# Kernel tuning notes

Measured on AMD Instinct MI355X. Metric: run time of the kernel, lower is better.

The kernel has to match this reference:

```python
import jax, jax.numpy as jnp
import numpy as np
import math

DIM = 512


def setup_inputs() -> dict:
    key = jax.random.key(0)
    ks = jax.random.split(key, 6)
    B, N, D = 4, 4096, DIM
    H = D // 2
    features = jax.random.normal(ks[0], (B, N, D), dtype=jnp.float32)
    W1 = jax.random.normal(ks[1], (D, H), dtype=jnp.float32) * 0.02
    b1 = jnp.zeros((H,), dtype=jnp.float32)
    ln_g = jnp.ones((H,), dtype=jnp.float32)
    ln_b = jnp.zeros((H,), dtype=jnp.float32)
    W2 = jax.random.normal(ks[2], (H, 1), dtype=jnp.float32) * 0.02
    b2 = jnp.zeros((1,), dtype=jnp.float32)
    target_entropy = jnp.ones((1,), dtype=jnp.float32) * math.log(D)
    temperature = jnp.ones((1,), dtype=jnp.float32)
    return {"features": features, "W1": W1, "b1": b1, "ln_g": ln_g,
            "ln_b": ln_b, "W2": W2, "b2": b2,
            "target_entropy": target_entropy, "temperature": temperature}


def _layernorm(x, g, b, eps=1e-5):
    mu = jnp.mean(x, axis=-1, keepdims=True)
    var = jnp.mean((x - mu) ** 2, axis=-1, keepdims=True)
    return (x - mu) * jax.lax.rsqrt(var + eps) * g + b


def reference(features, W1, b1, ln_g, ln_b, W2, b2, target_entropy, temperature):
    # ---- compute_entropy: pairwise RBF kernel over [B, N, D] ----
    sq = jnp.sum(features ** 2, axis=-1)                       # [B, N]
    gram = jnp.einsum('bnd,bmd->bnm', features, features)      # [B, N, N]
    d2 = jnp.maximum(sq[:, :, None] + sq[:, None, :] - 2.0 * gram, 0.0)
    tau = temperature[0]
    kernel = jnp.exp(-d2 / (2.0 * tau ** 2))                   # [B, N, N]
    probs = kernel / jnp.sum(kernel, axis=-1, keepdims=True)
    entropy = -jnp.sum(probs * jnp.log(probs + 1e-6), axis=-1)  # [B, N]

    # ---- entropy estimator MLP (computed in original forward, output unused) ----
    h = features @ W1 + b1
    h = _layernorm(h, ln_g, ln_b)
    h = jax.nn.gelu(h, approximate=False)
    estimated_entropy = h @ W2 + b2                            # [B, N, 1] (unused)
    del estimated_entropy

    # ---- sigmoid-gated control signal ----
    entropy_diff = entropy - target_entropy[0]
    control_signal = jax.nn.sigmoid(-entropy_diff / tau)       # [B, N]
    controlled_features = features * control_signal[..., None]
    return controlled_features, control_signal
```

## Files before the change

### kernel.cpp

```cpp
#include <hip/hip_runtime.h>
#include <stdint.h>

#define N_TOK 4096
#define DIM   512
#define BATCH 4
#define BN    (BATCH * N_TOK)
#define NSUP  16
#define NPAIR 136
#define IPW   64
#define IPB   256
#define NG2   16
#define SPG   2
#define NSP   (NG2 / SPG)

typedef __attribute__((ext_vector_type(4))) float f32x4;
typedef __attribute__((ext_vector_type(8))) int   i32x8;

typedef const __attribute__((address_space(1))) uint32_t* gptr_t;
typedef __attribute__((address_space(3))) uint32_t* lptr_t;

__device__ __forceinline__ float sumsq8(uint lo, uint hi) {
    float s = 0.f, f;
    f = __builtin_amdgcn_cvt_f32_fp8((int)lo, 0); s = fmaf(f, f, s);
    f = __builtin_amdgcn_cvt_f32_fp8((int)lo, 1); s = fmaf(f, f, s);
    f = __builtin_amdgcn_cvt_f32_fp8((int)lo, 2); s = fmaf(f, f, s);
    f = __builtin_amdgcn_cvt_f32_fp8((int)lo, 3); s = fmaf(f, f, s);
    f = __builtin_amdgcn_cvt_f32_fp8((int)hi, 0); s = fmaf(f, f, s);
    f = __builtin_amdgcn_cvt_f32_fp8((int)hi, 1); s = fmaf(f, f, s);
    f = __builtin_amdgcn_cvt_f32_fp8((int)hi, 2); s = fmaf(f, f, s);
    f = __builtin_amdgcn_cvt_f32_fp8((int)hi, 3); s = fmaf(f, f, s);
    return s;
}

__global__ __launch_bounds__(256) void prep_kernel(
    const float* __restrict__ feat, uint8_t* __restrict__ fbT,
    float* __restrict__ sq)
{
    __shared__ __align__(16) long lt[1024];
    const int t = threadIdx.x;
    const int row16 = t >> 4, seg = t & 15;
    const size_t grp = blockIdx.x;
    const size_t row = grp * 16 + row16;

    const float4* src = (const float4*)(feat + row * DIM + seg * 32);
    uint32_t wd[8];
    float s = 0.f;
#pragma unroll
    for (int i = 0; i < 4; ++i) {
        float4 a = src[2 * i], b = src[2 * i + 1];
        uint lo = (uint)__builtin_amdgcn_cvt_pk_fp8_f32(a.x, a.y, 0, false);
        lo      = (uint)__builtin_amdgcn_cvt_pk_fp8_f32(a.z, a.w, (int)lo, true);
        uint hi = (uint)__builtin_amdgcn_cvt_pk_fp8_f32(b.x, b.y, 0, false);
        hi      = (uint)__builtin_amdgcn_cvt_pk_fp8_f32(b.z, b.w, (int)hi, true);
        wd[2 * i] = lo; wd[2 * i + 1] = hi;
        s += sumsq8(lo, hi);
    }

#pragma unroll
    for (int i = 0; i < 4; ++i) {
        int c = seg * 4 + i;
        long d = ((long)(unsigned)wd[2 * i + 1] << 32) | (unsigned)wd[2 * i];
        lt[c * 16 + ((row16 + c) & 15)] = d;
    }

#pragma unroll
    for (int m = 1; m < 16; m <<= 1) s += __shfl_xor(s, m);
    if (seg == 0) sq[row] = s;

    __syncthreads();
    long* ot = (long*)(fbT + grp * 8192);
#pragma unroll
    for (int i = 0; i < 4; ++i) {
        int p    = t + i * 256;
        int kk   = p >> 8;
        int rem  = p & 255;
        int half = rem >> 7;
        int l6   = (rem >> 1) & 63;
        int qq   = l6 >> 4;
        int r    = l6 & 15;
        int w8   = half * 2 + (p & 1);
        int c    = kk * 16 + qq * 4 + w8;
        ot[p] = lt[c * 16 + ((r + c) & 15)];
    }
}

__global__ __launch_bounds__(256, 2) void entropy_kernel(
    const uint8_t* __restrict__ fbT,
    const float* __restrict__ sq, const float* __restrict__ temp,
    float* __restrict__ Sp, float* __restrict__ Tp)
{
    __shared__ uint4 buf[2][1024];
    __shared__ float sqlds[256];
    __shared__ float sjS[4][256];
    __shared__ float sjT[4][256];
    const int t    = threadIdx.x;
    const int w    = t >> 6;
    const int lane = t & 63;
    const int q    = lane >> 4;
    const int c16  = lane & 15;
    const int lbo  = lane * 16;

    const int flat  = blockIdx.x;
    const int batch = flat / NPAIR;
    int rem = flat - batch * NPAIR;
    int aa = 0;
    while (rem >= NSUP - aa) { rem -= NSUP - aa; ++aa; }
    const int bb = aa + rem;
    const int iw    = aa * IPB + w * IPW;
    const int jbase = bb * IPB;
    const size_t rowbase = (size_t)batch * N_TOK;

    const float tau    = temp[0];
    const float inv2t2 = 0.5f / (tau * tau);
    const float cg_    = 1.0f / (tau * tau);

#pragma unroll
    for (int i = 0; i < 4; ++i) { sjS[w][lane * 4 + i] = 0.f; sjT[w][lane * 4 + i] = 0.f; }

    i32x8 afrag[4][4];
#pragma unroll
    for (int s = 0; s < 4; ++s) {
        const uint8_t* ga = fbT + ((rowbase + iw) / 16 + s) * 8192;
#pragma unroll
        for (int kk = 0; kk < 4; ++kk) {
            uint4 lo = *(const uint4*)(ga + kk * 2048 + lbo);
            uint4 hi = *(const uint4*)(ga + kk * 2048 + 1024 + lbo);
            i32x8 v = {(int)lo.x, (int)lo.y, (int)lo.z, (int)lo.w,
                       (int)hi.x, (int)hi.y, (int)hi.z, (int)hi.w};
            afrag[s][kk] = v;
        }
    }
    float pi_[4][4];
    float pim = -1e30f;
#pragma unroll
    for (int s = 0; s < 4; ++s) {
        float4 p4 = *(const float4*)(sq + rowbase + iw + s * 16 + q * 4);
        pi_[s][0] = -p4.x * inv2t2; pi_[s][1] = -p4.y * inv2t2;
        pi_[s][2] = -p4.z * inv2t2; pi_[s][3] = -p4.w * inv2t2;
        pim = fmaxf(pim, fmaxf(fmaxf(pi_[s][0], pi_[s][1]),
                               fmaxf(pi_[s][2], pi_[s][3])));
    }
    sqlds[t] = sq[rowbase + jbase + t];

    float S[4][4], T[4][4];
#pragma unroll
    for (int s = 0; s < 4; ++s)
#pragma unroll
        for (int r = 0; r < 4; ++r) { S[s][r] = 0.f; T[s][r] = 0.f; }

    const uint8_t* bgbase = fbT
        + ((size_t)batch * (N_TOK / 16) + (size_t)(jbase / 16)) * 8192;

    auto stage_sp = [&](int sp, int b) {
#pragma unroll
        for (int i = 0; i < SPG; ++i) {
            const uint8_t* gs = bgbase + ((size_t)sp * SPG + i) * 8192 + w * 2048 + lbo;
            uint8_t* ld = (uint8_t*)(&buf[b][0]) + i * 8192 + w * 2048;
            __builtin_amdgcn_global_load_lds((gptr_t)(const void*)gs,
                                             (lptr_t)(void*)ld, 16, 0, 0);
            __builtin_amdgcn_global_load_lds((gptr_t)(const void*)(gs + 1024),
                                             (lptr_t)(void*)(ld + 1024), 16, 0, 0);
        }
    };

    stage_sp(0, 0);
    stage_sp(1, 1);
    asm volatile("s_waitcnt lgkmcnt(0)" ::: "memory");
    __builtin_amdgcn_s_barrier();

    for (int sp = 0; sp < NSP; ++sp) {
        if (sp < NSP - 1) asm volatile("s_waitcnt vmcnt(4)" ::: "memory");
        else              asm volatile("s_waitcnt vmcnt(0)" ::: "memory");
        __builtin_amdgcn_s_barrier();
        __builtin_amdgcn_sched_barrier(0);

        const uint8_t* sb = (const uint8_t*)(&buf[sp & 1][0]);
        __builtin_amdgcn_s_setprio(1);
#pragma unroll
        for (int i = 0; i < SPG; ++i) {
            const int g = sp * SPG + i;
            const uint8_t* bs = sb + i * 8192;
            float pj = -sqlds[g * 16 + c16] * inv2t2;
            f32x4 acc[4] = {{0,0,0,0},{0,0,0,0},{0,0,0,0},{0,0,0,0}};
#pragma unroll
            for (int kk = 0; kk < 4; ++kk) {
                uint4 lo = *(const uint4*)(bs + kk * 2048 + lbo);
                uint4 hi = *(const uint4*)(bs + kk * 2048 + 1024 + lbo);
                i32x8 b = {(int)lo.x, (int)lo.y, (int)lo.z, (int)lo.w,
                           (int)hi.x, (int)hi.y, (int)hi.z, (int)hi.w};
                acc[0] = __builtin_amdgcn_mfma_scale_f32_16x16x128_f8f6f4(afrag[0][kk], b, acc[0], 0, 0, 0, 127, 0, 127);
                acc[1] = __builtin_amdgcn_mfma_scale_f32_16x16x128_f8f6f4(afrag[1][kk], b, acc[1], 0, 0, 0, 127, 0, 127);
                acc[2] = __builtin_amdgcn_mfma_scale_f32_16x16x128_f8f6f4(afrag[2][kk], b, acc[2], 0, 0, 0, 127, 0, 127);
                acc[3] = __builtin_amdgcn_mfma_scale_f32_16x16x128_f8f6f4(afrag[3][kk], b, acc[3], 0, 0, 0, 127, 0, 127);
            }
            float m0 = fmaxf(fmaxf(acc[0][0], acc[0][1]), fmaxf(acc[0][2], acc[0][3]));
            float m1 = fmaxf(fmaxf(acc[1][0], acc[1][1]), fmaxf(acc[1][2], acc[1][3]));
            float m2 = fmaxf(fmaxf(acc[2][0], acc[2][1]), fmaxf(acc[2][2], acc[2][3]));
            float m3 = fmaxf(fmaxf(acc[3][0], acc[3][1]), fmaxf(acc[3][2], acc[3][3]));
            float mm = fmaxf(fmaxf(m0, m1), fmaxf(m2, m3));
            float bound = fmaf(mm, cg_, pim + pj);
            if (__any(bound > -110.0f)) {
                float ks = 0.f, kt = 0.f;
#pragma unroll
                for (int s = 0; s < 4; ++s)
#pragma unroll
                    for (int r = 0; r < 4; ++r) {
                        float e   = fmaf(acc[s][r], cg_, pi_[s][r] + pj);
                        float ee  = fminf(e, 0.f);
                        float k   = __expf(ee);
                        float kei = k * ee;
                        S[s][r] += k;  T[s][r] += kei;
                        ks      += k;  kt      += kei;
                    }
                if (aa != bb) {
                    ks += __shfl_xor(ks, 16); ks += __shfl_xor(ks, 32);
                    kt += __shfl_xor(kt, 16); kt += __shfl_xor(kt, 32);
                    if (lane < 16) {
                        sjS[w][g * 16 + lane] = ks;
                        sjT[w][g * 16 + lane] = kt;
                    }
                }
            }
        }
        __builtin_amdgcn_s_setprio(0);

        asm volatile("s_waitcnt lgkmcnt(0)" ::: "memory");
        __builtin_amdgcn_s_barrier();
        __builtin_amdgcn_sched_barrier(0);
        if (sp + 2 < NSP) stage_sp(sp + 2, sp & 1);
    }

#pragma unroll
    for (int m = 1; m < 16; m <<= 1)
#pragma unroll
        for (int s = 0; s < 4; ++s)
#pragma unroll
            for (int r = 0; r < 4; ++r) {
                S[s][r] += __shfl_xor(S[s][r], m);
                T[s][r] += __shfl_xor(T[s][r], m);
            }
    if (c16 == 0) {
#pragma unroll
        for (int s = 0; s < 4; ++s)
#pragma unroll
            for (int r = 0; r < 4; ++r) {
                size_t idx = (size_t)bb * BN + rowbase + iw + s * 16 + q * 4 + r;
                Sp[idx] = S[s][r];
                Tp[idx] = T[s][r];
            }
    }

    if (aa != bb) {
        __syncthreads();
        float s4 = sjS[0][t] + sjS[1][t] + sjS[2][t] + sjS[3][t];
        float t4 = sjT[0][t] + sjT[1][t] + sjT[2][t] + sjT[3][t];
        size_t idx = (size_t)aa * BN + rowbase + jbase + t;
        Sp[idx] = s4;
        Tp[idx] = t4;
    }
}

__global__ __launch_bounds__(256) void finalize_kernel(
    const float* __restrict__ feat, const float* __restrict__ Sp,
    const float* __restrict__ Tp, const float* __restrict__ tgt,
    const float* __restrict__ temp, float* __restrict__ out)
{
    int row  = (blockIdx.x << 2) + (threadIdx.x >> 6);
    int lane = threadIdx.x & 63;
    float S = 0.0f, T = 0.0f;
#pragma unroll
    for (int j = 0; j < NSUP; ++j) {
        S += Sp[(size_t)j * BN + row];
        T += Tp[(size_t)j * BN + row];
    }
    float tau = temp[0];
    float E  = __logf(S) - T / S;
    float cs = 1.0f / (1.0f + __expf((E - tgt[0]) / tau));

    const float4* F4 = (const float4*)(feat + (size_t)row * DIM);
    float4*       O4 = (float4*)(out + (size_t)row * DIM);
    float4 v0 = F4[lane], v1 = F4[lane + 64];
    v0.x *= cs; v0.y *= cs; v0.z *= cs; v0.w *= cs;
    v1.x *= cs; v1.y *= cs; v1.z *= cs; v1.w *= cs;
    O4[lane] = v0; O4[lane + 64] = v1;
    if (lane == 0) out[(size_t)BN * DIM + row] = cs;
}

extern "C" void kernel_launch(void* const* d_in, const int* in_sizes, int n_in,
                              void* d_out, int out_size, void* d_ws, size_t ws_size,
                              hipStream_t stream) {
    const float* feat = (const float*)d_in[0];
    const float* tgt  = (const float*)d_in[7];
    const float* temp = (const float*)d_in[8];
    float* out = (float*)d_out;

    char* ws = (char*)d_ws;
    uint8_t* fbT = (uint8_t*)ws;
    float*   sq  = (float*)(fbT + (size_t)BN * DIM);
    float*   Sp  = sq + BN;
    float*   Tp  = Sp + (size_t)NSUP * BN;

    prep_kernel<<<dim3(BN / 16), dim3(256), 0, stream>>>(feat, fbT, sq);
    entropy_kernel<<<dim3(BATCH * NPAIR), dim3(256), 0, stream>>>(fbT, sq, temp, Sp, Tp);
    finalize_kernel<<<dim3(BN / 4), dim3(256), 0, stream>>>(feat, Sp, Tp, tgt, temp, out);
}
```

Measured before the change: 139.7 us.

## Split each symmetric tile pair into two column halves to double grid size

Each entropy block now covers half of the 256-wide j range (128 columns), so the grid doubles from 544 to 1088 blocks. The goal is better load balance and occupancy across the MI355X CUs, since 544 blocks leave a ragged final wave. In exchange, every A-fragment load and prologue is paid twice as often, and the partial-sum buffers double to 32 slots, which adds finalize reads. Off-diagonal column sums are written to slot 2*aa, and slot 2*aa+1 is zero-filled.

```diff
diff --git a/kernel.cpp b/kernel.cpp
--- a/kernel.cpp
+++ b/kernel.cpp
@@ -9,9 +9,11 @@
 #define NPAIR 136
 #define IPW   64
 #define IPB   256
-#define NG2   16
+#define JPB   128
+#define NG2   8
 #define SPG   2
 #define NSP   (NG2 / SPG)
+#define NSLOT (2 * NSUP)
 
 typedef __attribute__((ext_vector_type(4))) float f32x4;
 typedef __attribute__((ext_vector_type(8))) int   i32x8;
@@ -90,9 +92,9 @@
     float* __restrict__ Sp, float* __restrict__ Tp)
 {
     __shared__ uint4 buf[2][1024];
-    __shared__ float sqlds[256];
-    __shared__ float sjS[4][256];
-    __shared__ float sjT[4][256];
+    __shared__ float sqlds[JPB];
+    __shared__ float sjS[4][JPB];
+    __shared__ float sjT[4][JPB];
     const int t    = threadIdx.x;
     const int w    = t >> 6;
     const int lane = t & 63;
@@ -101,21 +103,23 @@
     const int lbo  = lane * 16;
 
     const int flat  = blockIdx.x;
-    const int batch = flat / NPAIR;
-    int rem = flat - batch * NPAIR;
+    const int batch = flat / (NPAIR * 2);
+    int rem = flat - batch * (NPAIR * 2);
+    const int h = rem & 1;
+    rem >>= 1;
     int aa = 0;
     while (rem >= NSUP - aa) { rem -= NSUP - aa; ++aa; }
     const int bb = aa + rem;
     const int iw    = aa * IPB + w * IPW;
-    const int jbase = bb * IPB;
+    const int jbase = bb * IPB + h * JPB;
     const size_t rowbase = (size_t)batch * N_TOK;
 
     const float tau    = temp[0];
     const float inv2t2 = 0.5f / (tau * tau);
     const float cg_    = 1.0f / (tau * tau);
 
-#pragma unroll
-    for (int i = 0; i < 4; ++i) { sjS[w][lane * 4 + i] = 0.f; sjT[w][lane * 4 + i] = 0.f; }
+    sjS[w][lane] = 0.f; sjS[w][lane + 64] = 0.f;
+    sjT[w][lane] = 0.f; sjT[w][lane + 64] = 0.f;
 
     i32x8 afrag[4][4];
 #pragma unroll
@@ -140,7 +144,7 @@
         pim = fmaxf(pim, fmaxf(fmaxf(pi_[s][0], pi_[s][1]),
                                fmaxf(pi_[s][2], pi_[s][3])));
     }
-    sqlds[t] = sq[rowbase + jbase + t];
+    if (t < JPB) sqlds[t] = sq[rowbase + jbase + t];
 
     float S[4][4], T[4][4];
 #pragma unroll
@@ -244,7 +248,7 @@
         for (int s = 0; s < 4; ++s)
 #pragma unroll
             for (int r = 0; r < 4; ++r) {
-                size_t idx = (size_t)bb * BN + rowbase + iw + s * 16 + q * 4 + r;
+                size_t idx = (size_t)(2 * bb + h) * BN + rowbase + iw + s * 16 + q * 4 + r;
                 Sp[idx] = S[s][r];
                 Tp[idx] = T[s][r];
             }
@@ -252,11 +256,15 @@
 
     if (aa != bb) {
         __syncthreads();
-        float s4 = sjS[0][t] + sjS[1][t] + sjS[2][t] + sjS[3][t];
-        float t4 = sjT[0][t] + sjT[1][t] + sjT[2][t] + sjT[3][t];
-        size_t idx = (size_t)aa * BN + rowbase + jbase + t;
-        Sp[idx] = s4;
-        Tp[idx] = t4;
+        if (t < JPB) {
+            float s4 = sjS[0][t] + sjS[1][t] + sjS[2][t] + sjS[3][t];
+            float t4 = sjT[0][t] + sjT[1][t] + sjT[2][t] + sjT[3][t];
+            size_t row = rowbase + jbase + t;
+            Sp[(size_t)(2 * aa) * BN + row]     = s4;
+            Tp[(size_t)(2 * aa) * BN + row]     = t4;
+            Sp[(size_t)(2 * aa + 1) * BN + row] = 0.f;
+            Tp[(size_t)(2 * aa + 1) * BN + row] = 0.f;
+        }
     }
 }
 
@@ -269,7 +277,7 @@
     int lane = threadIdx.x & 63;
     float S = 0.0f, T = 0.0f;
 #pragma unroll
-    for (int j = 0; j < NSUP; ++j) {
+    for (int j = 0; j < NSLOT; ++j) {
         S += Sp[(size_t)j * BN + row];
         T += Tp[(size_t)j * BN + row];
     }
@@ -298,9 +306,9 @@
     uint8_t* fbT = (uint8_t*)ws;
     float*   sq  = (float*)(fbT + (size_t)BN * DIM);
     float*   Sp  = sq + BN;
-    float*   Tp  = Sp + (size_t)NSUP * BN;
+    float*   Tp  = Sp + (size_t)NSLOT * BN;
 
     prep_kernel<<<dim3(BN / 16), dim3(256), 0, stream>>>(feat, fbT, sq);
-    entropy_kernel<<<dim3(BATCH * NPAIR), dim3(256), 0, stream>>>(fbT, sq, temp, Sp, Tp);
+    entropy_kernel<<<dim3(BATCH * NPAIR * 2), dim3(256), 0, stream>>>(fbT, sq, temp, Sp, Tp);
     finalize_kernel<<<dim3(BN / 4), dim3(256), 0, stream>>>(feat, Sp, Tp, tgt, temp, out);
 }
```

Result: slower. 148.1 us (+6.0%).

## Split symmetric Gram work into equal-size chunks for better load balance

Applied to the files above, without the earlier changes.

Replaces the per-block 256x256 super-tile pairs (544 blocks) with 512 blocks that each process exactly 17 sixteen-column groups of the upper-triangular work, possibly spanning two row super-tiles. The goal is balanced work per block and a grid that divides evenly across the CUs, avoiding a tail wave. In exchange it needs 31 partial-sum slots, zeroing them in the prep kernel, and more reads in the finalize kernel. Each chunk segment also reloads its A fragments and adds barriers.

```diff
diff --git a/kernel.cpp b/kernel.cpp
--- a/kernel.cpp
+++ b/kernel.cpp
@@ -6,12 +6,10 @@
 #define BATCH 4
 #define BN    (BATCH * N_TOK)
 #define NSUP  16
-#define NPAIR 136
 #define IPW   64
 #define IPB   256
-#define NG2   16
-#define SPG   2
-#define NSP   (NG2 / SPG)
+#define CHUNK 17
+#define NSLOT 31
 
 typedef __attribute__((ext_vector_type(4))) float f32x4;
 typedef __attribute__((ext_vector_type(8))) int   i32x8;
@@ -34,13 +32,22 @@
 
 __global__ __launch_bounds__(256) void prep_kernel(
     const float* __restrict__ feat, uint8_t* __restrict__ fbT,
-    float* __restrict__ sq)
+    float* __restrict__ sq, float* __restrict__ Sp, float* __restrict__ Tp)
 {
     __shared__ __align__(16) long lt[1024];
     const int t = threadIdx.x;
     const int row16 = t >> 4, seg = t & 15;
     const size_t grp = blockIdx.x;
     const size_t row = grp * 16 + row16;
+
+    {
+        size_t idx = grp * 256 + t;
+        if (idx < (size_t)NSLOT * BN / 4) {
+            float4 z = {0.f, 0.f, 0.f, 0.f};
+            ((float4*)Sp)[idx] = z;
+            ((float4*)Tp)[idx] = z;
+        }
+    }
 
     const float4* src = (const float4*)(feat + row * DIM + seg * 32);
     uint32_t wd[8];
@@ -90,9 +97,9 @@
     float* __restrict__ Sp, float* __restrict__ Tp)
 {
     __shared__ uint4 buf[2][1024];
-    __shared__ float sqlds[256];
-    __shared__ float sjS[4][256];
-    __shared__ float sjT[4][256];
+    __shared__ float sqlds[288];
+    __shared__ float sjS[4][288];
+    __shared__ float sjT[4][288];
     const int t    = threadIdx.x;
     const int w    = t >> 6;
     const int lane = t & 63;
@@ -100,164 +107,182 @@
     const int c16  = lane & 15;
     const int lbo  = lane * 16;
 
-    const int flat  = blockIdx.x;
-    const int batch = flat / NPAIR;
-    int rem = flat - batch * NPAIR;
-    int aa = 0;
-    while (rem >= NSUP - aa) { rem -= NSUP - aa; ++aa; }
-    const int bb = aa + rem;
-    const int iw    = aa * IPB + w * IPW;
-    const int jbase = bb * IPB;
+    const int mb    = blockIdx.x & 127;
+    const int batch = blockIdx.x >> 7;
     const size_t rowbase = (size_t)batch * N_TOK;
 
     const float tau    = temp[0];
     const float inv2t2 = 0.5f / (tau * tau);
     const float cg_    = 1.0f / (tau * tau);
 
-#pragma unroll
-    for (int i = 0; i < 4; ++i) { sjS[w][lane * 4 + i] = 0.f; sjT[w][lane * 4 + i] = 0.f; }
-
-    i32x8 afrag[4][4];
-#pragma unroll
-    for (int s = 0; s < 4; ++s) {
-        const uint8_t* ga = fbT + ((rowbase + iw) / 16 + s) * 8192;
-#pragma unroll
-        for (int kk = 0; kk < 4; ++kk) {
-            uint4 lo = *(const uint4*)(ga + kk * 2048 + lbo);
-            uint4 hi = *(const uint4*)(ga + kk * 2048 + 1024 + lbo);
-            i32x8 v = {(int)lo.x, (int)lo.y, (int)lo.z, (int)lo.w,
-                       (int)hi.x, (int)hi.y, (int)hi.z, (int)hi.w};
-            afrag[s][kk] = v;
-        }
-    }
-    float pi_[4][4];
-    float pim = -1e30f;
-#pragma unroll
-    for (int s = 0; s < 4; ++s) {
-        float4 p4 = *(const float4*)(sq + rowbase + iw + s * 16 + q * 4);
-        pi_[s][0] = -p4.x * inv2t2; pi_[s][1] = -p4.y * inv2t2;
-        pi_[s][2] = -p4.z * inv2t2; pi_[s][3] = -p4.w * inv2t2;
-        pim = fmaxf(pim, fmaxf(fmaxf(pi_[s][0], pi_[s][1]),
-                               fmaxf(pi_[s][2], pi_[s][3])));
-    }
-    sqlds[t] = sq[rowbase + jbase + t];
-
-    float S[4][4], T[4][4];
-#pragma unroll
-    for (int s = 0; s < 4; ++s)
-#pragma unroll
-        for (int r = 0; r < 4; ++r) { S[s][r] = 0.f; T[s][r] = 0.f; }
-
-    const uint8_t* bgbase = fbT
-        + ((size_t)batch * (N_TOK / 16) + (size_t)(jbase / 16)) * 8192;
-
-    auto stage_sp = [&](int sp, int b) {
-#pragma unroll
-        for (int i = 0; i < SPG; ++i) {
-            const uint8_t* gs = bgbase + ((size_t)sp * SPG + i) * 8192 + w * 2048 + lbo;
-            uint8_t* ld = (uint8_t*)(&buf[b][0]) + i * 8192 + w * 2048;
-            __builtin_amdgcn_global_load_lds((gptr_t)(const void*)gs,
-                                             (lptr_t)(void*)ld, 16, 0, 0);
-            __builtin_amdgcn_global_load_lds((gptr_t)(const void*)(gs + 1024),
-                                             (lptr_t)(void*)(ld + 1024), 16, 0, 0);
-        }
-    };
-
-    stage_sp(0, 0);
-    stage_sp(1, 1);
-    asm volatile("s_waitcnt lgkmcnt(0)" ::: "memory");
-    __builtin_amdgcn_s_barrier();
-
-    for (int sp = 0; sp < NSP; ++sp) {
-        if (sp < NSP - 1) asm volatile("s_waitcnt vmcnt(4)" ::: "memory");
-        else              asm volatile("s_waitcnt vmcnt(0)" ::: "memory");
+    const int g0 = mb * CHUNK;
+    int a = 0, Ca = 0;
+    while (Ca + 16 * (NSUP - a) <= g0) { Ca += 16 * (NSUP - a); ++a; }
+    const int o      = g0 - Ca;
+    const int rowlen = 16 * (NSUP - a);
+    const int n1     = (rowlen - o < CHUNK) ? (rowlen - o) : CHUNK;
+
+    auto run_seg = [&](int aa, int CaX, int jjstart, int n) {
+        const int slot_i = mb - CaX / CHUNK;
+        const int iw = aa * IPB + w * IPW;
+
+        i32x8 afrag[4][4];
+#pragma unroll
+        for (int s = 0; s < 4; ++s) {
+            const uint8_t* ga = fbT + ((rowbase + iw) / 16 + s) * 8192;
+#pragma unroll
+            for (int kk = 0; kk < 4; ++kk) {
+                uint4 lo = *(const uint4*)(ga + kk * 2048 + lbo);
+                uint4 hi = *(const uint4*)(ga + kk * 2048 + 1024 + lbo);
+                i32x8 v = {(int)lo.x, (int)lo.y, (int)lo.z, (int)lo.w,
+                           (int)hi.x, (int)hi.y, (int)hi.z, (int)hi.w};
+                afrag[s][kk] = v;
+            }
+        }
+        float pi_[4][4];
+        float pim = -1e30f;
+#pragma unroll
+        for (int s = 0; s < 4; ++s) {
+            float4 p4 = *(const float4*)(sq + rowbase + iw + s * 16 + q * 4);
+            pi_[s][0] = -p4.x * inv2t2; pi_[s][1] = -p4.y * inv2t2;
+            pi_[s][2] = -p4.z * inv2t2; pi_[s][3] = -p4.w * inv2t2;
+            pim = fmaxf(pim, fmaxf(fmaxf(pi_[s][0], pi_[s][1]),
+                                   fmaxf(pi_[s][2], pi_[s][3])));
+        }
+        for (int idx = t; idx < n * 16; idx += 256)
+            sqlds[idx] = sq[rowbase + (size_t)jjstart * 16 + idx];
+        for (int idx = lane; idx < n * 16; idx += 64) {
+            sjS[w][idx] = 0.f; sjT[w][idx] = 0.f;
+        }
+
+        float S[4][4], T[4][4];
+#pragma unroll
+        for (int s = 0; s < 4; ++s)
+#pragma unroll
+            for (int r = 0; r < 4; ++r) { S[s][r] = 0.f; T[s][r] = 0.f; }
+
+        const uint8_t* bgbase = fbT
+            + ((size_t)batch * (N_TOK / 16) + (size_t)jjstart) * 8192;
+        const int NSPs = (n + 1) / 2;
+
+        auto stage_sp = [&](int sp, int b) {
+#pragma unroll
+            for (int i = 0; i < 2; ++i) {
+                int k = 2 * sp + i; if (k > n - 1) k = n - 1;
+                const uint8_t* gs = bgbase + (size_t)k * 8192 + w * 2048 + lbo;
+                uint8_t* ld = (uint8_t*)(&buf[b][0]) + i * 8192 + w * 2048;
+                __builtin_amdgcn_global_load_lds((gptr_t)(const void*)gs,
+                                                 (lptr_t)(void*)ld, 16, 0, 0);
+                __builtin_amdgcn_global_load_lds((gptr_t)(const void*)(gs + 1024),
+                                                 (lptr_t)(void*)(ld + 1024), 16, 0, 0);
+            }
+        };
+
+        asm volatile("s_waitcnt vmcnt(0) lgkmcnt(0)" ::: "memory");
         __builtin_amdgcn_s_barrier();
-        __builtin_amdgcn_sched_barrier(0);
-
-        const uint8_t* sb = (const uint8_t*)(&buf[sp & 1][0]);
-        __builtin_amdgcn_s_setprio(1);
-#pragma unroll
-        for (int i = 0; i < SPG; ++i) {
-            const int g = sp * SPG + i;
-            const uint8_t* bs = sb + i * 8192;
-            float pj = -sqlds[g * 16 + c16] * inv2t2;
-            f32x4 acc[4] = {{0,0,0,0},{0,0,0,0},{0,0,0,0},{0,0,0,0}};
-#pragma unroll
-            for (int kk = 0; kk < 4; ++kk) {
-                uint4 lo = *(const uint4*)(bs + kk * 2048 + lbo);
-                uint4 hi = *(const uint4*)(bs + kk * 2048 + 1024 + lbo);
-                i32x8 b = {(int)lo.x, (int)lo.y, (int)lo.z, (int)lo.w,
-                           (int)hi.x, (int)hi.y, (int)hi.z, (int)hi.w};
-                acc[0] = __builtin_amdgcn_mfma_scale_f32_16x16x128_f8f6f4(afrag[0][kk], b, acc[0], 0, 0, 0, 127, 0, 127);
-                acc[1] = __builtin_amdgcn_mfma_scale_f32_16x16x128_f8f6f4(afrag[1][kk], b, acc[1], 0, 0, 0, 127, 0, 127);
-                acc[2] = __builtin_amdgcn_mfma_scale_f32_16x16x128_f8f6f4(afrag[2][kk], b, acc[2], 0, 0, 0, 127, 0, 127);
-                acc[3] = __builtin_amdgcn_mfma_scale_f32_16x16x128_f8f6f4(afrag[3][kk], b, acc[3], 0, 0, 0, 127, 0, 127);
-            }
-            float m0 = fmaxf(fmaxf(acc[0][0], acc[0][1]), fmaxf(acc[0][2], acc[0][3]));
-            float m1 = fmaxf(fmaxf(acc[1][0], acc[1][1]), fmaxf(acc[1][2], acc[1][3]));
-            float m2 = fmaxf(fmaxf(acc[2][0], acc[2][1]), fmaxf(acc[2][2], acc[2][3]));
-            float m3 = fmaxf(fmaxf(acc[3][0], acc[3][1]), fmaxf(acc[3][2], acc[3][3]));
-            float mm = fmaxf(fmaxf(m0, m1), fmaxf(m2, m3));
-            float bound = fmaf(mm, cg_, pim + pj);
-            if (__any(bound > -110.0f)) {
-                float ks = 0.f, kt = 0.f;
-#pragma unroll
-                for (int s = 0; s < 4; ++s)
-#pragma unroll
-                    for (int r = 0; r < 4; ++r) {
-                        float e   = fmaf(acc[s][r], cg_, pi_[s][r] + pj);
-                        float ee  = fminf(e, 0.f);
-                        float k   = __expf(ee);
-                        float kei = k * ee;
-                        S[s][r] += k;  T[s][r] += kei;
-                        ks      += k;  kt      += kei;
-                    }
-                if (aa != bb) {
-                    ks += __shfl_xor(ks, 16); ks += __shfl_xor(ks, 32);
-                    kt += __shfl_xor(kt, 16); kt += __shfl_xor(kt, 32);
-                    if (lane < 16) {
-                        sjS[w][g * 16 + lane] = ks;
-                        sjT[w][g * 16 + lane] = kt;
+        stage_sp(0, 0);
+        if (NSPs > 1) stage_sp(1, 1);
+
+        for (int sp = 0; sp < NSPs; ++sp) {
+            if (sp + 2 <= NSPs) asm volatile("s_waitcnt vmcnt(4)" ::: "memory");
+            else                asm volatile("s_waitcnt vmcnt(0)" ::: "memory");
+            __builtin_amdgcn_s_barrier();
+            __builtin_amdgcn_sched_barrier(0);
+
+            const uint8_t* sb = (const uint8_t*)(&buf[sp & 1][0]);
+            __builtin_amdgcn_s_setprio(1);
+#pragma unroll
+            for (int i = 0; i < 2; ++i) {
+                const int k    = 2 * sp + i;
+                const int kr   = (k > n - 1) ? (n - 1) : k;
+                const bool dmy = (k > n - 1);
+                const uint8_t* bs = sb + i * 8192;
+                float pj = dmy ? -1e30f : -sqlds[kr * 16 + c16] * inv2t2;
+                f32x4 acc[4] = {{0,0,0,0},{0,0,0,0},{0,0,0,0},{0,0,0,0}};
+#pragma unroll
+                for (int kk = 0; kk < 4; ++kk) {
+                    uint4 lo = *(const uint4*)(bs + kk * 2048 + lbo);
+                    uint4 hi = *(const uint4*)(bs + kk * 2048 + 1024 + lbo);
+                    i32x8 b = {(int)lo.x, (int)lo.y, (int)lo.z, (int)lo.w,
+                               (int)hi.x, (int)hi.y, (int)hi.z, (int)hi.w};
+                    acc[0] = __builtin_amdgcn_mfma_scale_f32_16x16x128_f8f6f4(afrag[0][kk], b, acc[0], 0, 0, 0, 127, 0, 127);
+                    acc[1] = __builtin_amdgcn_mfma_scale_f32_16x16x128_f8f6f4(afrag[1][kk], b, acc[1], 0, 0, 0, 127, 0, 127);
+                    acc[2] = __builtin_amdgcn_mfma_scale_f32_16x16x128_f8f6f4(afrag[2][kk], b, acc[2], 0, 0, 0, 127, 0, 127);
+                    acc[3] = __builtin_amdgcn_mfma_scale_f32_16x16x128_f8f6f4(afrag[3][kk], b, acc[3], 0, 0, 0, 127, 0, 127);
+                }
+                float m0 = fmaxf(fmaxf(acc[0][0], acc[0][1]), fmaxf(acc[0][2], acc[0][3]));
+                float m1 = fmaxf(fmaxf(acc[1][0], acc[1][1]), fmaxf(acc[1][2], acc[1][3]));
+                float m2 = fmaxf(fmaxf(acc[2][0], acc[2][1]), fmaxf(acc[2][2], acc[2][3]));
+                float m3 = fmaxf(fmaxf(acc[3][0], acc[3][1]), fmaxf(acc[3][2], acc[3][3]));
+                float mm = fmaxf(fmaxf(m0, m1), fmaxf(m2, m3));
+                float bound = fmaf(mm, cg_, pim + pj);
+                if (__any(bound > -110.0f)) {
+                    float ks = 0.f, kt = 0.f;
+#pragma unroll
+                    for (int s = 0; s < 4; ++s)
+#pragma unroll
+                        for (int r = 0; r < 4; ++r) {
+                            float e   = fmaf(acc[s][r], cg_, pi_[s][r] + pj);
+                            float ee  = fminf(e, 0.f);
+                            float kv  = __expf(ee);
+                            float kei = kv * ee;
+                            S[s][r] += kv;  T[s][r] += kei;
+                            ks      += kv;  kt      += kei;
+                        }
+                    if (((jjstart + kr) >> 4) != aa) {
+                        ks += __shfl_xor(ks, 16); ks += __shfl_xor(ks, 32);
+                        kt += __shfl_xor(kt, 16); kt += __shfl_xor(kt, 32);
+                        if (lane < 16) {
+                            sjS[w][kr * 16 + lane] = ks;
+                            sjT[w][kr * 16 + lane] = kt;
+                        }
                     }
                 }
             }
-        }
-        __builtin_amdgcn_s_setprio(0);
-
-        asm volatile("s_waitcnt lgkmcnt(0)" ::: "memory");
-        __builtin_amdgcn_s_barrier();
-        __builtin_amdgcn_sched_barrier(0);
-        if (sp + 2 < NSP) stage_sp(sp + 2, sp & 1);
-    }
-
-#pragma unroll
-    for (int m = 1; m < 16; m <<= 1)
-#pragma unroll
-        for (int s = 0; s < 4; ++s)
-#pragma unroll
-            for (int r = 0; r < 4; ++r) {
-                S[s][r] += __shfl_xor(S[s][r], m);
-                T[s][r] += __shfl_xor(T[s][r], m);
+            __builtin_amdgcn_s_setprio(0);
+
+            asm volatile("s_waitcnt lgkmcnt(0)" ::: "memory");
+            __builtin_amdgcn_s_barrier();
+            __builtin_amdgcn_sched_barrier(0);
+            if (sp + 2 < NSPs) stage_sp(sp + 2, sp & 1);
+        }
+
+#pragma unroll
+        for (int m = 1; m < 16; m <<= 1)
+#pragma unroll
+            for (int s = 0; s < 4; ++s)
+#pragma unroll
+                for (int r = 0; r < 4; ++r) {
+                    S[s][r] += __shfl_xor(S[s][r], m);
+                    T[s][r] += __shfl_xor(T[s][r], m);
+                }
+        if (c16 == 0) {
+#pragma unroll
+            for (int s = 0; s < 4; ++s)
+#pragma unroll
+                for (int r = 0; r < 4; ++r) {
+                    size_t idx = (size_t)slot_i * BN + rowbase + iw + s * 16 + q * 4 + r;
+                    Sp[idx] = S[s][r];
+                    Tp[idx] = T[s][r];
+                }
+        }
+
+        __syncthreads();
+        for (int idx = t; idx < n * 16; idx += 256) {
+            int k = idx >> 4;
+            if (((jjstart + k) >> 4) != aa) {
+                float s4 = sjS[0][idx] + sjS[1][idx] + sjS[2][idx] + sjS[3][idx];
+                float t4 = sjT[0][idx] + sjT[1][idx] + sjT[2][idx] + sjT[3][idx];
+                size_t row = rowbase + (size_t)jjstart * 16 + idx;
+                Sp[(size_t)(16 + aa) * BN + row] = s4;
+                Tp[(size_t)(16 + aa) * BN + row] = t4;
             }
-    if (c16 == 0) {
-#pragma unroll
-        for (int s = 0; s < 4; ++s)
-#pragma unroll
-            for (int r = 0; r < 4; ++r) {
-                size_t idx = (size_t)bb * BN + rowbase + iw + s * 16 + q * 4 + r;
-                Sp[idx] = S[s][r];
-                Tp[idx] = T[s][r];
-            }
-    }
-
-    if (aa != bb) {
+        }
         __syncthreads();
-        float s4 = sjS[0][t] + sjS[1][t] + sjS[2][t] + sjS[3][t];
-        float t4 = sjT[0][t] + sjT[1][t] + sjT[2][t] + sjT[3][t];
-        size_t idx = (size_t)aa * BN + rowbase + jbase + t;
-        Sp[idx] = s4;
-        Tp[idx] = t4;
-    }
+    };
+
+    run_seg(a, Ca, a * 16 + o, n1);
+    if (n1 < CHUNK) run_seg(a + 1, Ca + rowlen, (a + 1) * 16, CHUNK - n1);
 }
 
 __global__ __launch_bounds__(256) void finalize_kernel(
@@ -269,7 +294,7 @@
     int lane = threadIdx.x & 63;
     float S = 0.0f, T = 0.0f;
 #pragma unroll
-    for (int j = 0; j < NSUP; ++j) {
+    for (int j = 0; j < NSLOT; ++j) {
         S += Sp[(size_t)j * BN + row];
         T += Tp[(size_t)j * BN + row];
     }
@@ -298,9 +323,9 @@
     uint8_t* fbT = (uint8_t*)ws;
     float*   sq  = (float*)(fbT + (size_t)BN * DIM);
     float*   Sp  = sq + BN;
-    float*   Tp  = Sp + (size_t)NSUP * BN;
-
-    prep_kernel<<<dim3(BN / 16), dim3(256), 0, stream>>>(feat, fbT, sq);
-    entropy_kernel<<<dim3(BATCH * NPAIR), dim3(256), 0, stream>>>(fbT, sq, temp, Sp, Tp);
+    float*   Tp  = Sp + (size_t)NSLOT * BN;
+
+    prep_kernel<<<dim3(BN / 16), dim3(256), 0, stream>>>(feat, fbT, sq, Sp, Tp);
+    entropy_kernel<<<dim3(BATCH * 128), dim3(256), 0, stream>>>(fbT, sq, temp, Sp, Tp);
     finalize_kernel<<<dim3(BN / 4), dim3(256), 0, stream>>>(feat, Sp, Tp, tgt, temp, out);
 }
```

Result: slower. 148.4 us (+6.2%).
